# Optimization experiments

Hardware: AMD Instinct MI355X
Metric: run time of the kernel (lower is better)

The kernel has to match this reference:

```python
import jax, jax.numpy as jnp
import numpy as np

KNN = 30
NUM_RBFS = 16
MIN_RBF, MAX_RBF = 2.0, 22.0
SPREAD = (MAX_RBF - MIN_RBF) / NUM_RBFS
D_MODEL = 128
A = 4                      # 3 backbone atoms + virtual (Ca+Cb) atom
E_DIM = NUM_RBFS * A * A   # 256, matches LayerNorm(num_rbfs*4*4)
Z, N = 2, 4096


def setup_inputs() -> dict:
    key = jax.random.key(0)
    k1, k2 = jax.random.split(key)
    # coords spread out so neighbor distances land across the RBF range [2, 22]
    C = jax.random.normal(k1, (Z, N, A, 3), jnp.float32) * 5.0
    node_mask = jnp.zeros((Z, N), bool)  # True = padded residue
    rbf_centers = jnp.linspace(MIN_RBF, MAX_RBF, NUM_RBFS).astype(jnp.float32)
    ln_gamma = jnp.ones((E_DIM,), jnp.float32)
    ln_beta = jnp.zeros((E_DIM,), jnp.float32)
    W = (jax.random.normal(k2, (E_DIM, D_MODEL), jnp.float32) / np.sqrt(E_DIM))
    b = jnp.zeros((D_MODEL,), jnp.float32)
    return {"C": C, "node_mask": node_mask, "rbf_centers": rbf_centers,
            "ln_gamma": ln_gamma, "ln_beta": ln_beta, "W": W, "b": b}


def _layernorm(x, g, b2, eps=1e-5):
    mu = jnp.mean(x, -1, keepdims=True)
    var = jnp.mean((x - mu) ** 2, -1, keepdims=True)
    return (x - mu) * jax.lax.rsqrt(var + eps) * g + b2


def _safe_dist(sq):
    pos = sq > 0
    return jnp.where(pos, jnp.sqrt(jnp.where(pos, sq, 1.0)), 0.0)


def _neighbors(Ca, node_mask):
    Zb, Nn, _ = Ca.shape
    # squared pairwise distances; topk on sq-dist == topk on dist (monotone)
    sq = jnp.sum((Ca[:, None, :, :] - Ca[:, :, None, :]) ** 2, -1)  # [Z,N,N]
    sq = jnp.where((sq == 0) | node_mask[:, :, None], jnp.inf, sq)
    neg, idx = jax.lax.top_k(-sq, KNN)  # K smallest
    sqv = -neg                           # squared topk distances
    nbr_mask = jnp.take_along_axis(
        jnp.broadcast_to(node_mask[:, :, None], (Zb, Nn, KNN)), idx, axis=1)
    # dist != 0 and dist < 12  <=>  sq != 0 and sq < 144
    edge_mask = (~(node_mask[:, :, None] | nbr_mask)) & (sqv != 0) & (sqv < 144.0)
    node_idxs = jnp.arange(Nn)[None, :, None]
    Kidx = jnp.where(edge_mask, idx, node_idxs)
    return Kidx, edge_mask


def _edges(C, Kidx, rbf_centers, ln_gamma, ln_beta, W, b):
    Zb, Nn, Kk = Kidx.shape
    CK = jax.vmap(lambda c, k: c[k])(C, Kidx)                     # [Z,N,K,A,3]
    diff = C[:, :, None, :, None, :] - CK[:, :, :, None, :, :]    # [Z,N,K,A,A,3]
    d = _safe_dist(jnp.sum(diff ** 2, -1))                        # [Z,N,K,A,A]
    rbf = jnp.exp(-((d[..., None] - rbf_centers) ** 2) / (SPREAD ** 2))
    E = rbf.reshape(Zb, Nn, Kk, -1)                               # [Z,N,K,256]
    return _layernorm(E, ln_gamma, ln_beta) @ W + b               # [Z,N,K,128]


def reference(C, node_mask, rbf_centers, ln_gamma, ln_beta, W, b):
    Ca = C[:, :, 1, :]  # alpha carbon
    Kidx, edge_mask = _neighbors(Ca, node_mask)
    E = _edges(C, Kidx, rbf_centers, ln_gamma, ln_beta, W, b)
    return E, Kidx, edge_mask
```

## Files before the change

### kernel.cpp

```cpp
#include <hip/hip_runtime.h>
#include <math.h>

#define ZB 2
#define NN 4096
#define KNNv 30
#define EDIM 256
#define DM 128
#define BINS 4096
#define CAP 2048

typedef __attribute__((ext_vector_type(8))) short bf16x8;
typedef __attribute__((ext_vector_type(4))) float fx4;

#define ELN_STR 264

static __device__ inline unsigned short f2bf(float f) {
    unsigned int u = __float_as_uint(f);
    unsigned int r = u + 0x7fffu + ((u >> 16) & 1u);
    return (unsigned short)(r >> 16);
}

__global__ __launch_bounds__(256) void caprep_kernel(
    const float* __restrict__ C, float4* __restrict__ Ca4)
{
    int tid = blockIdx.x * 256 + threadIdx.x;
    if (tid < ZB * NN) {
        const float* p = C + (size_t)tid * 12 + 3;
        Ca4[tid] = make_float4(p[0], p[1], p[2], 0.0f);
    }
}

__global__ __launch_bounds__(256) void wprep_kernel(
    const float* __restrict__ W, const float* __restrict__ gamma_,
    unsigned short* __restrict__ Wt)
{
    int base = blockIdx.x * 1024 + threadIdx.x;
    #pragma unroll
    for (int q = 0; q < 4; ++q) {
        int idx = base + q * 256;
        int k = idx >> 7, n = idx & 127;
        Wt[n * 256 + k] = f2bf(W[idx] * gamma_[k]);
    }
}

__global__ __launch_bounds__(128) void biasprep_kernel(
    const float* __restrict__ W, const float* __restrict__ beta_,
    const float* __restrict__ bias, float* __restrict__ bias2)
{
    int n = threadIdx.x;
    float acc = bias[n];
    #pragma unroll 8
    for (int k = 0; k < EDIM; ++k) acc += beta_[k] * W[k * 128 + n];
    bias2[n] = acc;
}

__global__ __launch_bounds__(256) void knn_kernel(
    const float4* __restrict__ Ca4,
    const unsigned char* __restrict__ node_mask,
    float* __restrict__ out_kidx,
    float* __restrict__ out_emask)
{
    __shared__ unsigned int hist[BINS];
    __shared__ unsigned long long buf[CAP];
    __shared__ unsigned int wsum[4];
    __shared__ int s_cut;
    __shared__ unsigned int s_m;
    __shared__ unsigned long long sel[KNNv];

    const int bi = blockIdx.x;
    const int z  = bi >> 12;
    const int i  = bi & (NN - 1);
    const int t  = threadIdx.x;

    for (int q = t; q < BINS; q += 256) hist[q] = 0u;
    if (t == 0) s_m = 0u;
    __syncthreads();

    const float4 me = Ca4[bi];
    const float xi = me.x, yi = me.y, zi = me.z;
    const bool mask_i = node_mask[bi] != 0;
    const float4* Cz = Ca4 + ((size_t)z << 12);

    unsigned int keys[16];
    #pragma unroll
    for (int q = 0; q < 16; ++q) {
        const int j = q * 256 + t;
        float4 p = Cz[j];
        float dx = p.x - xi, dy = p.y - yi, dz = p.z - zi;
        float s = dx * dx + dy * dy + dz * dz;
        if (s == 0.0f || mask_i) s = __builtin_inff();
        unsigned int k = __float_as_uint(s);
        keys[q] = k;
        atomicAdd(&hist[k >> 20], 1u);
    }
    __syncthreads();

    unsigned int cnt[16]; unsigned int Tsum = 0;
    #pragma unroll
    for (int q = 0; q < 16; ++q) { cnt[q] = hist[t * 16 + q]; Tsum += cnt[q]; }
    unsigned int incl = Tsum;
    #pragma unroll
    for (int off = 1; off < 64; off <<= 1) {
        unsigned int v = __shfl_up(incl, off);
        if ((t & 63) >= off) incl += v;
    }
    if ((t & 63) == 63) wsum[t >> 6] = incl;
    __syncthreads();
    unsigned int woff = 0;
    for (int w = 0; w < (t >> 6); ++w) woff += wsum[w];
    unsigned int run = woff + incl - Tsum;
    #pragma unroll
    for (int q = 0; q < 16; ++q) {
        unsigned int c = cnt[q];
        if (run < KNNv && run + c >= KNNv) s_cut = t * 16 + q;
        run += c;
    }
    __syncthreads();

    const int cutbin = s_cut;
    #pragma unroll
    for (int q = 0; q < 16; ++q) {
        unsigned int k = keys[q];
        if ((int)(k >> 20) <= cutbin) {
            unsigned int pos = atomicAdd(&s_m, 1u);
            if (pos < CAP)
                buf[pos] = ((unsigned long long)k << 32) | (unsigned int)(q * 256 + t);
        }
    }
    __syncthreads();
    unsigned int M = s_m; if (M > CAP) M = CAP;

    for (unsigned int c = t; c < M; c += 256) {
        unsigned long long mev = buf[c];
        unsigned int r = 0;
        for (unsigned int o = 0; o < M; ++o) r += (buf[o] < mev) ? 1u : 0u;
        if (r < KNNv) sel[r] = mev;
    }
    __syncthreads();

    if (t < KNNv) {
        unsigned long long p = sel[t];
        unsigned int k = (unsigned int)(p >> 32);
        int j = (int)(p & 0xffffffffu);
        float sv = __uint_as_float(k);
        bool nb = node_mask[(size_t)z * NN + j] != 0;
        bool em = (!mask_i && !nb) && (sv != 0.0f) && (sv < 144.0f);
        int kv = em ? j : i;
        size_t o = (size_t)bi * KNNv + t;
        out_kidx[o]  = (float)kv;
        out_emask[o] = em ? 1.0f : 0.0f;
    }
}

__global__ __launch_bounds__(256) void edge_kernel(
    const float* __restrict__ C,
    const float* __restrict__ kidxf,
    const float* __restrict__ centers,
    const unsigned short* __restrict__ Wt,
    const float* __restrict__ bias2,
    float* __restrict__ outE)
{
    __shared__ unsigned short Eln[64 * ELN_STR];
    const int t = threadIdx.x;
    const long g0 = (long)blockIdx.x * 64;

    {
        const int e   = t >> 2;
        const int sub = t & 3;
        const long g = g0 + e;
        const int z   = (int)(g / (NN * KNNv));
        const int rem = (int)(g - (long)z * NN * KNNv);
        const int i   = rem / KNNv;
        const int j   = (int)kidxf[g];

        const float* Ci = C + (((size_t)z * NN + i) * 4 + sub) * 3;
        const float ax = Ci[0], ay = Ci[1], az = Ci[2];
        const float* Cj = C + ((size_t)z * NN + j) * 12;
        float d[4];
        #pragma unroll
        for (int b = 0; b < 4; ++b) {
            float dx = ax - Cj[b * 3 + 0];
            float dy = ay - Cj[b * 3 + 1];
            float dz = az - Cj[b * 3 + 2];
            float s = dx * dx + dy * dy + dz * dz;
            d[b] = s > 0.0f ? sqrtf(s) : 0.0f;
        }
        float cen[16];
        #pragma unroll
        for (int r = 0; r < 16; ++r) cen[r] = centers[r];

        float vals[64];
        float sum = 0.f, sumsq = 0.f;
        #pragma unroll
        for (int b = 0; b < 4; ++b) {
            #pragma unroll
            for (int r = 0; r < 16; ++r) {
                float dd = d[b] - cen[r];
                float v = __expf(dd * dd * -0.64f);
                vals[b * 16 + r] = v;
                sum += v; sumsq += v * v;
            }
        }
        sum   += __shfl_xor(sum, 1);   sum   += __shfl_xor(sum, 2);
        sumsq += __shfl_xor(sumsq, 1); sumsq += __shfl_xor(sumsq, 2);
        const float mu   = sum * (1.0f / 256.0f);
        const float var  = sumsq * (1.0f / 256.0f) - mu * mu;
        const float rstd = rsqrtf(var + 1e-5f);
        #pragma unroll
        for (int w = 0; w < 8; ++w) {
            bf16x8 pk;
            #pragma unroll
            for (int v = 0; v < 8; ++v)
                pk[v] = (short)f2bf((vals[w * 8 + v] - mu) * rstd);
            *(bf16x8*)&Eln[e * ELN_STR + sub * 64 + w * 8] = pk;
        }
    }
    __syncthreads();

    {
        const int lane = t & 63;
        const int wv   = t >> 6;
        const int quad = lane >> 4;
        const int l15  = lane & 15;
        const int n0   = wv * 32;

        bf16x8 Bf[2][8];
        #pragma unroll
        for (int nt = 0; nt < 2; ++nt)
            #pragma unroll
            for (int ks = 0; ks < 8; ++ks)
                Bf[nt][ks] = *(const bf16x8*)(Wt + (size_t)(n0 + nt * 16 + l15) * 256
                                                 + ks * 32 + quad * 8);

        fx4 acc[4][2];
        #pragma unroll
        for (int mt = 0; mt < 4; ++mt)
            #pragma unroll
            for (int nt = 0; nt < 2; ++nt)
                acc[mt][nt] = (fx4){0.f, 0.f, 0.f, 0.f};

        #pragma unroll
        for (int ks = 0; ks < 8; ++ks) {
            bf16x8 Af[4];
            #pragma unroll
            for (int mt = 0; mt < 4; ++mt)
                Af[mt] = *(const bf16x8*)&Eln[(mt * 16 + l15) * ELN_STR + ks * 32 + quad * 8];
            #pragma unroll
            for (int mt = 0; mt < 4; ++mt) {
                acc[mt][0] = __builtin_amdgcn_mfma_f32_16x16x32_bf16(Af[mt], Bf[0][ks], acc[mt][0], 0, 0, 0);
                acc[mt][1] = __builtin_amdgcn_mfma_f32_16x16x32_bf16(Af[mt], Bf[1][ks], acc[mt][1], 0, 0, 0);
            }
        }

        const float bb0 = bias2[n0 + l15];
        const float bb1 = bias2[n0 + 16 + l15];
        #pragma unroll
        for (int mt = 0; mt < 4; ++mt) {
            #pragma unroll
            for (int r = 0; r < 4; ++r) {
                const long row = g0 + mt * 16 + quad * 4 + r;
                float* orow = outE + (size_t)row * DM;
                orow[n0 + l15]      = acc[mt][0][r] + bb0;
                orow[n0 + 16 + l15] = acc[mt][1][r] + bb1;
            }
        }
    }
}

extern "C" void kernel_launch(void* const* d_in, const int* in_sizes, int n_in,
                              void* d_out, int out_size, void* d_ws, size_t ws_size,
                              hipStream_t stream) {
    const float* C          = (const float*)d_in[0];
    const unsigned char* nm = (const unsigned char*)d_in[1];
    const float* centers    = (const float*)d_in[2];
    const float* gamma_     = (const float*)d_in[3];
    const float* beta_      = (const float*)d_in[4];
    const float* W          = (const float*)d_in[5];
    const float* bias       = (const float*)d_in[6];

    float* out = (float*)d_out;
    const size_t nE = (size_t)ZB * NN * KNNv * DM;
    const size_t nK = (size_t)ZB * NN * KNNv;
    float* outE = out;
    float* outK = out + nE;
    float* outM = outK + nK;

    unsigned short* Wt   = (unsigned short*)d_ws;
    float*          bias2 = (float*)((char*)d_ws + 65536);
    float4*         Ca4  = (float4*)((char*)d_ws + 66048);

    caprep_kernel<<<32, 256, 0, stream>>>(C, Ca4);
    wprep_kernel<<<32, 256, 0, stream>>>(W, gamma_, Wt);
    biasprep_kernel<<<1, 128, 0, stream>>>(W, beta_, bias, bias2);
    knn_kernel<<<ZB * NN, 256, 0, stream>>>(Ca4, nm, outK, outM);
    edge_kernel<<<(int)(nK / 64), 256, 0, stream>>>(C, outK, centers, Wt, bias2, outE);
}
```

Baseline: 243.9 us.

## Restructure kNN to one wavefront per two query nodes with packed histograms

The kNN kernel now gives each wavefront two query nodes, with 8 nodes per 256-thread block. Each wavefront keeps a private 2048-bin shared histogram that packs both nodes' counts into 16-bit halves, so the cutoff scan and candidate selection run inside the wave with shuffles and ballots instead of block-wide barriers. Distances are recomputed in the selection pass rather than held in registers, and the candidate buffer per node shrinks to 256. The edge kernel also loads neighbour coordinates as three float4 vectors, and the launch order moves kNN before the weight prep kernels. Risks are the coarser bins and the smaller candidate cap: a cutoff bin holding more than 256 candidates would drop true neighbours.

```diff
diff --git a/kernel.cpp b/kernel.cpp
--- a/kernel.cpp
+++ b/kernel.cpp
@@ -6,8 +6,8 @@
 #define KNNv 30
 #define EDIM 256
 #define DM 128
-#define BINS 4096
-#define CAP 2048
+#define HBINS 2048
+#define CAPW 256
 
 typedef __attribute__((ext_vector_type(8))) short bf16x8;
 typedef __attribute__((ext_vector_type(4))) float fx4;
@@ -54,101 +54,132 @@
     bias2[n] = acc;
 }
 
+static __device__ inline void keys2(float4 p, float4 c0, float4 c1,
+                                    bool m0, bool m1,
+                                    unsigned int& k0, unsigned int& k1)
+{
+    float dx0 = p.x - c0.x, dy0 = p.y - c0.y, dz0 = p.z - c0.z;
+    float s0 = dx0 * dx0 + dy0 * dy0 + dz0 * dz0;
+    if (s0 == 0.0f || m0) s0 = __builtin_inff();
+    k0 = __float_as_uint(s0);
+    float dx1 = p.x - c1.x, dy1 = p.y - c1.y, dz1 = p.z - c1.z;
+    float s1 = dx1 * dx1 + dy1 * dy1 + dz1 * dz1;
+    if (s1 == 0.0f || m1) s1 = __builtin_inff();
+    k1 = __float_as_uint(s1);
+}
+
 __global__ __launch_bounds__(256) void knn_kernel(
     const float4* __restrict__ Ca4,
     const unsigned char* __restrict__ node_mask,
     float* __restrict__ out_kidx,
     float* __restrict__ out_emask)
 {
-    __shared__ unsigned int hist[BINS];
-    __shared__ unsigned long long buf[CAP];
-    __shared__ unsigned int wsum[4];
-    __shared__ int s_cut;
-    __shared__ unsigned int s_m;
-    __shared__ unsigned long long sel[KNNv];
-
-    const int bi = blockIdx.x;
-    const int z  = bi >> 12;
-    const int i  = bi & (NN - 1);
-    const int t  = threadIdx.x;
-
-    for (int q = t; q < BINS; q += 256) hist[q] = 0u;
-    if (t == 0) s_m = 0u;
+    __shared__ unsigned int hist[4][HBINS];
+    __shared__ unsigned long long buf[4][2][CAPW];
+    __shared__ unsigned int mcnt[4][2];
+
+    const int t = threadIdx.x;
+    const int wv = t >> 6, lane = t & 63;
+    const int node0 = (blockIdx.x * 4 + wv) * 2;
+    const int z = node0 >> 12;
+
+    {
+        uint4* hz = (uint4*)&hist[wv][lane * 32];
+        #pragma unroll
+        for (int q = 0; q < 8; ++q) hz[q] = make_uint4(0u, 0u, 0u, 0u);
+        if (lane < 2) mcnt[wv][lane] = 0u;
+    }
+
+    const float4 c0 = Ca4[node0];
+    const float4 c1 = Ca4[node0 + 1];
+    const bool m0 = node_mask[node0] != 0;
+    const bool m1 = node_mask[node0 + 1] != 0;
+    const float4* Cz = Ca4 + ((size_t)z << 12);
     __syncthreads();
 
-    const float4 me = Ca4[bi];
-    const float xi = me.x, yi = me.y, zi = me.z;
-    const bool mask_i = node_mask[bi] != 0;
-    const float4* Cz = Ca4 + ((size_t)z << 12);
-
-    unsigned int keys[16];
-    #pragma unroll
-    for (int q = 0; q < 16; ++q) {
-        const int j = q * 256 + t;
-        float4 p = Cz[j];
-        float dx = p.x - xi, dy = p.y - yi, dz = p.z - zi;
-        float s = dx * dx + dy * dy + dz * dz;
-        if (s == 0.0f || mask_i) s = __builtin_inff();
-        unsigned int k = __float_as_uint(s);
-        keys[q] = k;
-        atomicAdd(&hist[k >> 20], 1u);
+    #pragma unroll 4
+    for (int q = 0; q < 64; ++q) {
+        float4 p = Cz[q * 64 + lane];
+        unsigned int k0, k1;
+        keys2(p, c0, c1, m0, m1, k0, k1);
+        atomicAdd(&hist[wv][k0 >> 21], 1u);
+        atomicAdd(&hist[wv][k1 >> 21], 0x10000u);
     }
     __syncthreads();
 
-    unsigned int cnt[16]; unsigned int Tsum = 0;
-    #pragma unroll
-    for (int q = 0; q < 16; ++q) { cnt[q] = hist[t * 16 + q]; Tsum += cnt[q]; }
-    unsigned int incl = Tsum;
+    uint4 ch[8];
+    unsigned int lsum = 0;
+    {
+        const uint4* hp = (const uint4*)&hist[wv][lane * 32];
+        #pragma unroll
+        for (int q = 0; q < 8; ++q) {
+            ch[q] = hp[q];
+            lsum += ch[q].x + ch[q].y + ch[q].z + ch[q].w;
+        }
+    }
+    unsigned int incl = lsum;
     #pragma unroll
     for (int off = 1; off < 64; off <<= 1) {
         unsigned int v = __shfl_up(incl, off);
-        if ((t & 63) >= off) incl += v;
-    }
-    if ((t & 63) == 63) wsum[t >> 6] = incl;
+        if (lane >= off) incl += v;
+    }
+    const unsigned int excl = incl - lsum;
+
+    int cutl = -1, cuth = -1;
+    {
+        unsigned int run_lo = excl & 0xffffu, run_hi = excl >> 16;
+        #pragma unroll
+        for (int q = 0; q < 32; ++q) {
+            unsigned int pk = ((const unsigned int*)ch)[q];
+            unsigned int clo = pk & 0xffffu, chi = pk >> 16;
+            if (run_lo < KNNv && run_lo + clo >= KNNv) cutl = lane * 32 + q;
+            if (run_hi < KNNv && run_hi + chi >= KNNv) cuth = lane * 32 + q;
+            run_lo += clo; run_hi += chi;
+        }
+    }
+    unsigned long long b0 = __ballot(cutl >= 0);
+    unsigned long long b1 = __ballot(cuth >= 0);
+    const int cut0 = __shfl(cutl, (int)__builtin_ctzll(b0));
+    const int cut1 = __shfl(cuth, (int)__builtin_ctzll(b1));
+
+    #pragma unroll 2
+    for (int q = 0; q < 64; ++q) {
+        const int j = q * 64 + lane;
+        float4 p = Cz[j];
+        unsigned int k0, k1;
+        keys2(p, c0, c1, m0, m1, k0, k1);
+        if ((int)(k0 >> 21) <= cut0) {
+            unsigned int pos = atomicAdd(&mcnt[wv][0], 1u);
+            if (pos < CAPW) buf[wv][0][pos] = ((unsigned long long)k0 << 32) | (unsigned int)j;
+        }
+        if ((int)(k1 >> 21) <= cut1) {
+            unsigned int pos = atomicAdd(&mcnt[wv][1], 1u);
+            if (pos < CAPW) buf[wv][1][pos] = ((unsigned long long)k1 << 32) | (unsigned int)j;
+        }
+    }
     __syncthreads();
-    unsigned int woff = 0;
-    for (int w = 0; w < (t >> 6); ++w) woff += wsum[w];
-    unsigned int run = woff + incl - Tsum;
+
     #pragma unroll
-    for (int q = 0; q < 16; ++q) {
-        unsigned int c = cnt[q];
-        if (run < KNNv && run + c >= KNNv) s_cut = t * 16 + q;
-        run += c;
-    }
-    __syncthreads();
-
-    const int cutbin = s_cut;
-    #pragma unroll
-    for (int q = 0; q < 16; ++q) {
-        unsigned int k = keys[q];
-        if ((int)(k >> 20) <= cutbin) {
-            unsigned int pos = atomicAdd(&s_m, 1u);
-            if (pos < CAP)
-                buf[pos] = ((unsigned long long)k << 32) | (unsigned int)(q * 256 + t);
-        }
-    }
-    __syncthreads();
-    unsigned int M = s_m; if (M > CAP) M = CAP;
-
-    for (unsigned int c = t; c < M; c += 256) {
-        unsigned long long mev = buf[c];
-        unsigned int r = 0;
-        for (unsigned int o = 0; o < M; ++o) r += (buf[o] < mev) ? 1u : 0u;
-        if (r < KNNv) sel[r] = mev;
-    }
-    __syncthreads();
-
-    if (t < KNNv) {
-        unsigned long long p = sel[t];
-        unsigned int k = (unsigned int)(p >> 32);
-        int j = (int)(p & 0xffffffffu);
-        float sv = __uint_as_float(k);
-        bool nb = node_mask[(size_t)z * NN + j] != 0;
-        bool em = (!mask_i && !nb) && (sv != 0.0f) && (sv < 144.0f);
-        int kv = em ? j : i;
-        size_t o = (size_t)bi * KNNv + t;
-        out_kidx[o]  = (float)kv;
-        out_emask[o] = em ? 1.0f : 0.0f;
+    for (int h = 0; h < 2; ++h) {
+        const int bi = node0 + h;
+        const bool mi = h ? m1 : m0;
+        unsigned int M = mcnt[wv][h]; if (M > CAPW) M = CAPW;
+        for (unsigned int c = lane; c < M; c += 64) {
+            unsigned long long me = buf[wv][h][c];
+            unsigned int r = 0;
+            for (unsigned int o = 0; o < M; ++o) r += (buf[wv][h][o] < me) ? 1u : 0u;
+            if (r < KNNv) {
+                unsigned int k = (unsigned int)(me >> 32);
+                int j = (int)(me & 0xffffffffu);
+                float sv = __uint_as_float(k);
+                bool nb = node_mask[((size_t)z << 12) + j] != 0;
+                bool em = (!mi && !nb) && (sv != 0.0f) && (sv < 144.0f);
+                int kv = em ? j : (bi & (NN - 1));
+                size_t o = (size_t)bi * KNNv + r;
+                out_kidx[o]  = (float)kv;
+                out_emask[o] = em ? 1.0f : 0.0f;
+            }
+        }
     }
 }
 
@@ -175,13 +206,16 @@
 
         const float* Ci = C + (((size_t)z * NN + i) * 4 + sub) * 3;
         const float ax = Ci[0], ay = Ci[1], az = Ci[2];
-        const float* Cj = C + ((size_t)z * NN + j) * 12;
+        const float4* Cj4 = (const float4*)(C + ((size_t)z * NN + j) * 12);
+        float4 q0 = Cj4[0], q1 = Cj4[1], q2 = Cj4[2];
+        const float bx[4] = {q0.x, q0.w, q1.z, q2.y};
+        const float by[4] = {q0.y, q1.x, q1.w, q2.z};
+        const float bz[4] = {q0.z, q1.y, q2.x, q2.w};
+
         float d[4];
         #pragma unroll
         for (int b = 0; b < 4; ++b) {
-            float dx = ax - Cj[b * 3 + 0];
-            float dy = ay - Cj[b * 3 + 1];
-            float dz = az - Cj[b * 3 + 2];
+            float dx = ax - bx[b], dy = ay - by[b], dz = az - bz[b];
             float s = dx * dx + dy * dy + dz * dz;
             d[b] = s > 0.0f ? sqrtf(s) : 0.0f;
         }
@@ -285,13 +319,13 @@
     float* outK = out + nE;
     float* outM = outK + nK;
 
-    unsigned short* Wt   = (unsigned short*)d_ws;
+    unsigned short* Wt    = (unsigned short*)d_ws;
     float*          bias2 = (float*)((char*)d_ws + 65536);
-    float4*         Ca4  = (float4*)((char*)d_ws + 66048);
+    float4*         Ca4   = (float4*)((char*)d_ws + 66048);
 
     caprep_kernel<<<32, 256, 0, stream>>>(C, Ca4);
+    knn_kernel<<<ZB * NN / 8, 256, 0, stream>>>(Ca4, nm, outK, outM);
     wprep_kernel<<<32, 256, 0, stream>>>(W, gamma_, Wt);
     biasprep_kernel<<<1, 128, 0, stream>>>(W, beta_, bias, bias2);
-    knn_kernel<<<ZB * NN, 256, 0, stream>>>(Ca4, nm, outK, outM);
     edge_kernel<<<(int)(nK / 64), 256, 0, stream>>>(C, outK, centers, Wt, bias2, outE);
 }
```

After: 262.1 us. +7.4%, slower.
